# Optimization experiments

Measured on AMD Instinct MI355X. Metric: run time of the kernel, lower is better.

Reference implementation:

```python
import jax, jax.numpy as jnp
import numpy as np

EPS = 1e-8  # matches torch.nn.functional.cosine_similarity default eps


def setup_inputs() -> dict:
    key = jax.random.key(0)
    k1, k2 = jax.random.split(key)
    B, C, L, D = 65536, 64, 64, 128
    x = jax.random.normal(k1, (B, D), dtype=jnp.float32)
    category_embeddings = jax.random.normal(k2, (C, L, D), dtype=jnp.float32)
    leaf_usage_counts = jnp.zeros((C, L), dtype=jnp.float32)
    return {
        "x": x,
        "category_embeddings": category_embeddings,
        "leaf_usage_counts": leaf_usage_counts,
    }


def reference(x, category_embeddings, leaf_usage_counts):
    # Cosine similarity: [B, C, L] without materializing the broadcast [B,C,L,D].
    x_norm = jnp.maximum(jnp.linalg.norm(x, axis=-1, keepdims=True), EPS)        # [B, 1]
    e_norm = jnp.maximum(jnp.linalg.norm(category_embeddings, axis=-1), EPS)     # [C, L]
    dots = jnp.einsum('bd,cld->bcl', x, category_embeddings)                     # [B, C, L]
    cosine_sim = dots / (x_norm[:, :, None] * e_norm[None, :, :])                # [B, C, L]

    # Training-path usage-count update (done under no_grad in torch):
    # per-category bincount of argmax leaf, scatter-added into the buffer.
    max_indices = jnp.argmax(cosine_sim, axis=2)                                 # [B, C] int
    C, L = leaf_usage_counts.shape
    cat_ids = jnp.broadcast_to(jnp.arange(C)[None, :], max_indices.shape)        # [B, C]
    leaf_counts = jnp.zeros((C, L), jnp.float32).at[cat_ids, max_indices].add(1.0)
    new_leaf_usage_counts = leaf_usage_counts + leaf_counts                      # [C, L]

    cosine_sim_max = jnp.max(cosine_sim, axis=2)                                 # [B, C]
    return cosine_sim_max, new_leaf_usage_counts
```

## Files before the change

kernel.cpp:

```cpp
#include <hip/hip_runtime.h>
#include <stdint.h>
#include <stddef.h>

#define D      128
#define NCATS  64
#define NLEAF  64
#define NC_BLK 32
#define BM     256
#define BIAS   32.0f

typedef _Float16 half8_t  __attribute__((ext_vector_type(8)));
typedef _Float16 half4h_t __attribute__((ext_vector_type(4)));
typedef float    float4_t __attribute__((ext_vector_type(4)));

__device__ __forceinline__ void async_ld16(const void* g, void* l) {
  __builtin_amdgcn_global_load_lds((const __attribute__((address_space(1))) uint32_t*)g,
                                   (__attribute__((address_space(3))) uint32_t*)l,
                                   16, 0, 0);
}

#define UMAX(a, b) ((a) > (b) ? (a) : (b))
#define DPP_REDUCE16(p)                                                                   \
  do {                                                                                    \
    unsigned _t;                                                                          \
    _t = (unsigned)__builtin_amdgcn_mov_dpp((int)(p), 0x121, 0xf, 0xf, false); p = UMAX(p, _t); \
    _t = (unsigned)__builtin_amdgcn_mov_dpp((int)(p), 0x122, 0xf, 0xf, false); p = UMAX(p, _t); \
    _t = (unsigned)__builtin_amdgcn_mov_dpp((int)(p), 0x124, 0xf, 0xf, false); p = UMAX(p, _t); \
    _t = (unsigned)__builtin_amdgcn_mov_dpp((int)(p), 0x128, 0xf, 0xf, false); p = UMAX(p, _t); \
  } while (0)

__global__ __launch_bounds__(256) void prep_e_kernel(const float* __restrict__ e,
                                                     char* __restrict__ e16) {
  const int t  = threadIdx.x;
  const int rl = t >> 4;
  const int cc = t & 15;
  const int row = blockIdx.x * 16 + rl;
  const float* src = e + (size_t)row * D + cc * 8;
  float4_t v0 = *(const float4_t*)src;
  float4_t v1 = *(const float4_t*)(src + 4);
  float ss = v0.x*v0.x + v0.y*v0.y + v0.z*v0.z + v0.w*v0.w +
             v1.x*v1.x + v1.y*v1.y + v1.z*v1.z + v1.w*v1.w;
  ss += __shfl_xor(ss, 1);
  ss += __shfl_xor(ss, 2);
  ss += __shfl_xor(ss, 4);
  ss += __shfl_xor(ss, 8);
  const float inv = 1.0f / fmaxf(sqrtf(ss), 1e-8f);
  half8_t h;
  h[0] = (_Float16)(v0.x * inv); h[1] = (_Float16)(v0.y * inv);
  h[2] = (_Float16)(v0.z * inv); h[3] = (_Float16)(v0.w * inv);
  h[4] = (_Float16)(v1.x * inv); h[5] = (_Float16)(v1.y * inv);
  h[6] = (_Float16)(v1.z * inv); h[7] = (_Float16)(v1.w * inv);
  const int dc = cc ^ (rl & 7);
  *(half8_t*)(e16 + (size_t)row * 256 + dc * 16) = h;
}

__global__ __launch_bounds__(256) void init_counts_kernel(const float* __restrict__ in,
                                                          float* __restrict__ out) {
  const int i = blockIdx.x * 256 + threadIdx.x;
  out[i] = in[i];
}

__global__ __launch_bounds__(256, 2) void main_kernel(const float* __restrict__ x,
                                                      const char* __restrict__ e16,
                                                      float* __restrict__ cos_out,
                                                      float* __restrict__ counts_out) {
  __shared__ __align__(16) char ebuf[2][16384];
  __shared__ unsigned hist[NC_BLK * NLEAF];
  __shared__ _Float16 stage[BM * 36];

  const int tid  = threadIdx.x;
  const int w    = tid >> 6;
  const int lane = tid & 63;
  const int q    = lane >> 4;
  const int wl   = lane & 15;

  const int rb     = blockIdx.x >> 1;
  const int c_base = (blockIdx.x & 1) * NC_BLK;
  const int b_base = rb * BM;

  for (int i = tid; i < NC_BLK * NLEAF; i += 256) hist[i] = 0;

  {
    const char* g = e16 + (size_t)c_base * 16384 + w * 4096 + lane * 16;
    char* l = &ebuf[0][w * 4096 + lane * 16];
#pragma unroll
    for (int j = 0; j < 4; ++j) async_ld16(g + j * 1024, l + j * 1024);
  }

  half8_t a[4][4];
  float inv_x[4];
#pragma unroll
  for (int rt = 0; rt < 4; ++rt) {
    const int row = b_base + w * 64 + rt * 16 + wl;
    const float* xr = x + (size_t)row * D;
    float ss = 0.f;
#pragma unroll
    for (int s = 0; s < 4; ++s) {
      const float* p = xr + s * 32 + q * 8;
      float4_t v0 = *(const float4_t*)p;
      float4_t v1 = *(const float4_t*)(p + 4);
      half8_t h;
      h[0] = (_Float16)v0.x; h[1] = (_Float16)v0.y;
      h[2] = (_Float16)v0.z; h[3] = (_Float16)v0.w;
      h[4] = (_Float16)v1.x; h[5] = (_Float16)v1.y;
      h[6] = (_Float16)v1.z; h[7] = (_Float16)v1.w;
      a[rt][s] = h;
      ss += v0.x*v0.x + v0.y*v0.y + v0.z*v0.z + v0.w*v0.w +
            v1.x*v1.x + v1.y*v1.y + v1.z*v1.z + v1.w*v1.w;
    }
    ss += __shfl_xor(ss, 16);
    ss += __shfl_xor(ss, 32);
    inv_x[rt] = 1.0f / fmaxf(sqrtf(ss), 1e-8f);
  }

  int rowbase[4], xoff[4];
#pragma unroll
  for (int nt = 0; nt < 4; ++nt) rowbase[nt] = (nt * 16 + wl) * 256;
#pragma unroll
  for (int s = 0; s < 4; ++s) xoff[s] = ((q + 4 * s) ^ (wl & 7)) * 16;

  unsigned idxv[4];
#pragma unroll
  for (int nt = 0; nt < 4; ++nt) idxv[nt] = (unsigned)(nt * 16 + wl);

  const float4_t bias4 = {BIAS, BIAS, BIAS, BIAS};

  __syncthreads();

#pragma unroll 2
  for (int ci = 0; ci < NC_BLK; ++ci) {
    const int c = c_base + ci;
    const char* cur = ebuf[ci & 1];

    if (ci + 1 < NC_BLK) {
      const char* g = e16 + (size_t)(c + 1) * 16384 + w * 4096 + lane * 16;
      char* l = &ebuf[(ci + 1) & 1][w * 4096 + lane * 16];
#pragma unroll
      for (int j = 0; j < 4; ++j) async_ld16(g + j * 1024, l + j * 1024);
    }

    float4_t acc[4][4];
#pragma unroll
    for (int s = 0; s < 4; ++s) {
      half8_t b[4];
#pragma unroll
      for (int nt = 0; nt < 4; ++nt)
        b[nt] = *(const half8_t*)(cur + rowbase[nt] + xoff[s]);
#pragma unroll
      for (int rt = 0; rt < 4; ++rt)
#pragma unroll
        for (int nt = 0; nt < 4; ++nt)
          acc[rt][nt] = __builtin_amdgcn_mfma_f32_16x16x32_f16(
              a[rt][s], b[nt], (s == 0) ? bias4 : acc[rt][nt], 0, 0, 0);
    }

    unsigned pk[4][4];
#pragma unroll
    for (int rt = 0; rt < 4; ++rt) {
#pragma unroll
      for (int reg = 0; reg < 4; ++reg) {
        unsigned k0 = (__float_as_uint(acc[rt][0][reg]) & 0xFFFFFFC0u) | idxv[0];
        unsigned k1 = (__float_as_uint(acc[rt][1][reg]) & 0xFFFFFFC0u) | idxv[1];
        unsigned k2 = (__float_as_uint(acc[rt][2][reg]) & 0xFFFFFFC0u) | idxv[2];
        unsigned k3 = (__float_as_uint(acc[rt][3][reg]) & 0xFFFFFFC0u) | idxv[3];
        unsigned p = UMAX(UMAX(k0, k1), UMAX(k2, k3));
        DPP_REDUCE16(p);
        pk[rt][reg] = p;
      }
    }

    if ((wl >> 2) == q) {
      const int reg = wl & 3;
#pragma unroll
      for (int rt = 0; rt < 4; ++rt) {
        const unsigned p = pk[rt][reg];
        const float val = (__uint_as_float(p & 0xFFFFFFC0u) - BIAS) * inv_x[rt];
        stage[(w * 64 + rt * 16 + wl) * 36 + ci] = (_Float16)val;
        atomicAdd(&hist[ci * NLEAF + (int)(p & 63u)], 1u);
      }
    }
    __syncthreads();
  }

  __syncthreads();

#pragma unroll
  for (int k = 0; k < 8; ++k) {
    const int r  = (tid >> 3) + 32 * k;
    const int c0 = (tid & 7) * 4;
    half4h_t h = *(const half4h_t*)&stage[r * 36 + c0];
    float4_t v;
    v.x = (float)h[0]; v.y = (float)h[1]; v.z = (float)h[2]; v.w = (float)h[3];
    *(float4_t*)&cos_out[(size_t)(b_base + r) * NCATS + c_base + c0] = v;
  }

  for (int i = tid; i < NC_BLK * NLEAF; i += 256) {
    const unsigned v = hist[i];
    if (v) atomicAdd(&counts_out[c_base * NLEAF + i], (float)v);
  }
}

extern "C" void kernel_launch(void* const* d_in, const int* in_sizes, int n_in,
                              void* d_out, int out_size, void* d_ws, size_t ws_size,
                              hipStream_t stream) {
  const float* x   = (const float*)d_in[0];
  const float* e   = (const float*)d_in[1];
  const float* cin = (const float*)d_in[2];

  const int B = in_sizes[0] / D;
  const int erows = in_sizes[1] / D;
  float* cos_out = (float*)d_out;
  float* counts_out = cos_out + (size_t)B * NCATS;
  char* e16 = (char*)d_ws;

  prep_e_kernel<<<erows / 16, 256, 0, stream>>>(e, e16);
  init_counts_kernel<<<(NCATS * NLEAF) / 256, 256, 0, stream>>>(cin, counts_out);
  main_kernel<<<(B / BM) * 2, 256, 0, stream>>>(x, e16, cos_out, counts_out);
}
```

Before: 163.4 us.

## Load embedding fragments directly from global memory, split categories four ways, merge init kernel

The main kernel no longer double-buffers embedding tiles in LDS with async global-to-LDS loads and per-category barriers. Each lane now reads its B fragments straight from global memory, relying on L2/L1 caching of the small fp16 embedding table. Categories are split into four blocks of 16 per row tile, which doubles the grid and the number of times each x tile is loaded and converted. Dropping the big LDS buffer allows an occupancy hint of 3 blocks per CU, and the counts-copy kernel is folded into the prep kernel to save a launch.

```diff
diff --git a/kernel.cpp b/kernel.cpp
--- a/kernel.cpp
+++ b/kernel.cpp
@@ -5,19 +5,13 @@
 #define D      128
 #define NCATS  64
 #define NLEAF  64
-#define NC_BLK 32
+#define NC_BLK 16
 #define BM     256
 #define BIAS   32.0f
 
 typedef _Float16 half8_t  __attribute__((ext_vector_type(8)));
 typedef _Float16 half4h_t __attribute__((ext_vector_type(4)));
 typedef float    float4_t __attribute__((ext_vector_type(4)));
-
-__device__ __forceinline__ void async_ld16(const void* g, void* l) {
-  __builtin_amdgcn_global_load_lds((const __attribute__((address_space(1))) uint32_t*)g,
-                                   (__attribute__((address_space(3))) uint32_t*)l,
-                                   16, 0, 0);
-}
 
 #define UMAX(a, b) ((a) > (b) ? (a) : (b))
 #define DPP_REDUCE16(p)                                                                   \
@@ -30,7 +24,9 @@
   } while (0)
 
 __global__ __launch_bounds__(256) void prep_e_kernel(const float* __restrict__ e,
-                                                     char* __restrict__ e16) {
+                                                     char* __restrict__ e16,
+                                                     const float* __restrict__ cin,
+                                                     float* __restrict__ counts_out) {
   const int t  = threadIdx.x;
   const int rl = t >> 4;
   const int cc = t & 15;
@@ -50,23 +46,17 @@
   h[2] = (_Float16)(v0.z * inv); h[3] = (_Float16)(v0.w * inv);
   h[4] = (_Float16)(v1.x * inv); h[5] = (_Float16)(v1.y * inv);
   h[6] = (_Float16)(v1.z * inv); h[7] = (_Float16)(v1.w * inv);
-  const int dc = cc ^ (rl & 7);
-  *(half8_t*)(e16 + (size_t)row * 256 + dc * 16) = h;
+  *(half8_t*)(e16 + (size_t)row * 256 + cc * 16) = h;
+  if (blockIdx.x < (NCATS * NLEAF) / 256)
+    counts_out[blockIdx.x * 256 + t] = cin[blockIdx.x * 256 + t];
 }
 
-__global__ __launch_bounds__(256) void init_counts_kernel(const float* __restrict__ in,
-                                                          float* __restrict__ out) {
-  const int i = blockIdx.x * 256 + threadIdx.x;
-  out[i] = in[i];
-}
-
-__global__ __launch_bounds__(256, 2) void main_kernel(const float* __restrict__ x,
+__global__ __launch_bounds__(256, 3) void main_kernel(const float* __restrict__ x,
                                                       const char* __restrict__ e16,
                                                       float* __restrict__ cos_out,
                                                       float* __restrict__ counts_out) {
-  __shared__ __align__(16) char ebuf[2][16384];
   __shared__ unsigned hist[NC_BLK * NLEAF];
-  __shared__ _Float16 stage[BM * 36];
+  __shared__ __align__(16) _Float16 stage[BM * 20];
 
   const int tid  = threadIdx.x;
   const int w    = tid >> 6;
@@ -74,18 +64,11 @@
   const int q    = lane >> 4;
   const int wl   = lane & 15;
 
-  const int rb     = blockIdx.x >> 1;
-  const int c_base = (blockIdx.x & 1) * NC_BLK;
+  const int rb     = blockIdx.x >> 2;
+  const int c_base = (blockIdx.x & 3) * NC_BLK;
   const int b_base = rb * BM;
 
   for (int i = tid; i < NC_BLK * NLEAF; i += 256) hist[i] = 0;
-
-  {
-    const char* g = e16 + (size_t)c_base * 16384 + w * 4096 + lane * 16;
-    char* l = &ebuf[0][w * 4096 + lane * 16];
-#pragma unroll
-    for (int j = 0; j < 4; ++j) async_ld16(g + j * 1024, l + j * 1024);
-  }
 
   half8_t a[4][4];
   float inv_x[4];
@@ -113,39 +96,24 @@
     inv_x[rt] = 1.0f / fmaxf(sqrtf(ss), 1e-8f);
   }
 
-  int rowbase[4], xoff[4];
-#pragma unroll
-  for (int nt = 0; nt < 4; ++nt) rowbase[nt] = (nt * 16 + wl) * 256;
-#pragma unroll
-  for (int s = 0; s < 4; ++s) xoff[s] = ((q + 4 * s) ^ (wl & 7)) * 16;
-
   unsigned idxv[4];
 #pragma unroll
   for (int nt = 0; nt < 4; ++nt) idxv[nt] = (unsigned)(nt * 16 + wl);
 
   const float4_t bias4 = {BIAS, BIAS, BIAS, BIAS};
 
+  const char* ebase = e16 + (size_t)c_base * 16384 + wl * 256 + q * 16;
+
   __syncthreads();
 
-#pragma unroll 2
   for (int ci = 0; ci < NC_BLK; ++ci) {
-    const int c = c_base + ci;
-    const char* cur = ebuf[ci & 1];
-
-    if (ci + 1 < NC_BLK) {
-      const char* g = e16 + (size_t)(c + 1) * 16384 + w * 4096 + lane * 16;
-      char* l = &ebuf[(ci + 1) & 1][w * 4096 + lane * 16];
-#pragma unroll
-      for (int j = 0; j < 4; ++j) async_ld16(g + j * 1024, l + j * 1024);
-    }
-
     float4_t acc[4][4];
 #pragma unroll
     for (int s = 0; s < 4; ++s) {
       half8_t b[4];
 #pragma unroll
       for (int nt = 0; nt < 4; ++nt)
-        b[nt] = *(const half8_t*)(cur + rowbase[nt] + xoff[s]);
+        b[nt] = *(const half8_t*)(ebase + nt * 4096 + s * 64);
 #pragma unroll
       for (int rt = 0; rt < 4; ++rt)
 #pragma unroll
@@ -153,6 +121,7 @@
           acc[rt][nt] = __builtin_amdgcn_mfma_f32_16x16x32_f16(
               a[rt][s], b[nt], (s == 0) ? bias4 : acc[rt][nt], 0, 0, 0);
     }
+    ebase += 16384;
 
     unsigned pk[4][4];
 #pragma unroll
@@ -175,20 +144,20 @@
       for (int rt = 0; rt < 4; ++rt) {
         const unsigned p = pk[rt][reg];
         const float val = (__uint_as_float(p & 0xFFFFFFC0u) - BIAS) * inv_x[rt];
-        stage[(w * 64 + rt * 16 + wl) * 36 + ci] = (_Float16)val;
+        stage[(w * 64 + rt * 16 + wl) * 20 + ci] = (_Float16)val;
         atomicAdd(&hist[ci * NLEAF + (int)(p & 63u)], 1u);
       }
     }
-    __syncthreads();
   }
 
   __syncthreads();
 
 #pragma unroll
-  for (int k = 0; k < 8; ++k) {
-    const int r  = (tid >> 3) + 32 * k;
-    const int c0 = (tid & 7) * 4;
-    half4h_t h = *(const half4h_t*)&stage[r * 36 + c0];
+  for (int k = 0; k < 4; ++k) {
+    const int id = k * 256 + tid;
+    const int r  = id >> 2;
+    const int c0 = (id & 3) * 4;
+    half4h_t h = *(const half4h_t*)&stage[r * 20 + c0];
     float4_t v;
     v.x = (float)h[0]; v.y = (float)h[1]; v.z = (float)h[2]; v.w = (float)h[3];
     *(float4_t*)&cos_out[(size_t)(b_base + r) * NCATS + c_base + c0] = v;
@@ -213,7 +182,6 @@
   float* counts_out = cos_out + (size_t)B * NCATS;
   char* e16 = (char*)d_ws;
 
-  prep_e_kernel<<<erows / 16, 256, 0, stream>>>(e, e16);
-  init_counts_kernel<<<(NCATS * NLEAF) / 256, 256, 0, stream>>>(cin, counts_out);
-  main_kernel<<<(B / BM) * 2, 256, 0, stream>>>(x, e16, cos_out, counts_out);
+  prep_e_kernel<<<erows / 16, 256, 0, stream>>>(e, e16, cin, counts_out);
+  main_kernel<<<(B / BM) * (NCATS / NC_BLK), 256, 0, stream>>>(x, e16, cos_out, counts_out);
 }
```

Result: slower. 332.4 us (+103.5%).

## Split categories finer per block, shrink accumulators, and fuse count init into prep

Applied to the files above, without the earlier changes.

Each block now handles 8 categories instead of 32, so the grid grows fourfold. The GEMM loop now processes one N-tile at a time with a running max, which cuts live accumulator registers and allows launch bounds of 3 blocks per SIMD. The count-buffer initialization is folded into the prep kernel, removing one launch. The trade-off is that every x tile is reloaded and converted to fp16 eight times instead of twice, which adds global traffic and prologue work per block.

```diff
diff --git a/kernel.cpp b/kernel.cpp
--- a/kernel.cpp
+++ b/kernel.cpp
@@ -5,7 +5,7 @@
 #define D      128
 #define NCATS  64
 #define NLEAF  64
-#define NC_BLK 32
+#define NC_BLK 8
 #define BM     256
 #define BIAS   32.0f
 
@@ -30,7 +30,9 @@
   } while (0)
 
 __global__ __launch_bounds__(256) void prep_e_kernel(const float* __restrict__ e,
-                                                     char* __restrict__ e16) {
+                                                     char* __restrict__ e16,
+                                                     const float* __restrict__ cin,
+                                                     float* __restrict__ counts_out) {
   const int t  = threadIdx.x;
   const int rl = t >> 4;
   const int cc = t & 15;
@@ -52,21 +54,17 @@
   h[6] = (_Float16)(v1.z * inv); h[7] = (_Float16)(v1.w * inv);
   const int dc = cc ^ (rl & 7);
   *(half8_t*)(e16 + (size_t)row * 256 + dc * 16) = h;
-}
-
-__global__ __launch_bounds__(256) void init_counts_kernel(const float* __restrict__ in,
-                                                          float* __restrict__ out) {
-  const int i = blockIdx.x * 256 + threadIdx.x;
-  out[i] = in[i];
-}
-
-__global__ __launch_bounds__(256, 2) void main_kernel(const float* __restrict__ x,
+  if (blockIdx.x < (NCATS * NLEAF) / 256)
+    counts_out[blockIdx.x * 256 + t] = cin[blockIdx.x * 256 + t];
+}
+
+__global__ __launch_bounds__(256, 3) void main_kernel(const float* __restrict__ x,
                                                       const char* __restrict__ e16,
                                                       float* __restrict__ cos_out,
                                                       float* __restrict__ counts_out) {
   __shared__ __align__(16) char ebuf[2][16384];
   __shared__ unsigned hist[NC_BLK * NLEAF];
-  __shared__ _Float16 stage[BM * 36];
+  __shared__ __align__(16) _Float16 stage[BM * 12];
 
   const int tid  = threadIdx.x;
   const int w    = tid >> 6;
@@ -74,8 +72,8 @@
   const int q    = lane >> 4;
   const int wl   = lane & 15;
 
-  const int rb     = blockIdx.x >> 1;
-  const int c_base = (blockIdx.x & 1) * NC_BLK;
+  const int rb     = blockIdx.x >> 3;
+  const int c_base = (blockIdx.x & 7) * NC_BLK;
   const int b_base = rb * BM;
 
   for (int i = tid; i < NC_BLK * NLEAF; i += 256) hist[i] = 0;
@@ -119,55 +117,46 @@
 #pragma unroll
   for (int s = 0; s < 4; ++s) xoff[s] = ((q + 4 * s) ^ (wl & 7)) * 16;
 
-  unsigned idxv[4];
-#pragma unroll
-  for (int nt = 0; nt < 4; ++nt) idxv[nt] = (unsigned)(nt * 16 + wl);
-
   const float4_t bias4 = {BIAS, BIAS, BIAS, BIAS};
 
   __syncthreads();
 
-#pragma unroll 2
   for (int ci = 0; ci < NC_BLK; ++ci) {
-    const int c = c_base + ci;
     const char* cur = ebuf[ci & 1];
 
     if (ci + 1 < NC_BLK) {
-      const char* g = e16 + (size_t)(c + 1) * 16384 + w * 4096 + lane * 16;
+      const char* g = e16 + (size_t)(c_base + ci + 1) * 16384 + w * 4096 + lane * 16;
       char* l = &ebuf[(ci + 1) & 1][w * 4096 + lane * 16];
 #pragma unroll
       for (int j = 0; j < 4; ++j) async_ld16(g + j * 1024, l + j * 1024);
     }
 
-    float4_t acc[4][4];
-#pragma unroll
-    for (int s = 0; s < 4; ++s) {
-      half8_t b[4];
-#pragma unroll
-      for (int nt = 0; nt < 4; ++nt)
-        b[nt] = *(const half8_t*)(cur + rowbase[nt] + xoff[s]);
+    unsigned pk[4][4];
+#pragma unroll
+    for (int nt = 0; nt < 4; ++nt) {
+      float4_t acc[4];
+#pragma unroll
+      for (int s = 0; s < 4; ++s) {
+        half8_t b = *(const half8_t*)(cur + rowbase[nt] + xoff[s]);
+#pragma unroll
+        for (int rt = 0; rt < 4; ++rt)
+          acc[rt] = __builtin_amdgcn_mfma_f32_16x16x32_f16(
+              a[rt][s], b, (s == 0) ? bias4 : acc[rt], 0, 0, 0);
+      }
+      const unsigned idc = (unsigned)(nt * 16 + wl);
 #pragma unroll
       for (int rt = 0; rt < 4; ++rt)
 #pragma unroll
-        for (int nt = 0; nt < 4; ++nt)
-          acc[rt][nt] = __builtin_amdgcn_mfma_f32_16x16x32_f16(
-              a[rt][s], b[nt], (s == 0) ? bias4 : acc[rt][nt], 0, 0, 0);
-    }
-
-    unsigned pk[4][4];
-#pragma unroll
-    for (int rt = 0; rt < 4; ++rt) {
-#pragma unroll
-      for (int reg = 0; reg < 4; ++reg) {
-        unsigned k0 = (__float_as_uint(acc[rt][0][reg]) & 0xFFFFFFC0u) | idxv[0];
-        unsigned k1 = (__float_as_uint(acc[rt][1][reg]) & 0xFFFFFFC0u) | idxv[1];
-        unsigned k2 = (__float_as_uint(acc[rt][2][reg]) & 0xFFFFFFC0u) | idxv[2];
-        unsigned k3 = (__float_as_uint(acc[rt][3][reg]) & 0xFFFFFFC0u) | idxv[3];
-        unsigned p = UMAX(UMAX(k0, k1), UMAX(k2, k3));
-        DPP_REDUCE16(p);
-        pk[rt][reg] = p;
-      }
-    }
+        for (int reg = 0; reg < 4; ++reg) {
+          unsigned k = (__float_as_uint(acc[rt][reg]) & 0xFFFFFFC0u) | idc;
+          pk[rt][reg] = (nt == 0) ? k : UMAX(pk[rt][reg], k);
+        }
+    }
+
+#pragma unroll
+    for (int rt = 0; rt < 4; ++rt)
+#pragma unroll
+      for (int reg = 0; reg < 4; ++reg) DPP_REDUCE16(pk[rt][reg]);
 
     if ((wl >> 2) == q) {
       const int reg = wl & 3;
@@ -175,7 +164,7 @@
       for (int rt = 0; rt < 4; ++rt) {
         const unsigned p = pk[rt][reg];
         const float val = (__uint_as_float(p & 0xFFFFFFC0u) - BIAS) * inv_x[rt];
-        stage[(w * 64 + rt * 16 + wl) * 36 + ci] = (_Float16)val;
+        stage[(w * 64 + rt * 16 + wl) * 12 + ci] = (_Float16)val;
         atomicAdd(&hist[ci * NLEAF + (int)(p & 63u)], 1u);
       }
     }
@@ -185,10 +174,11 @@
   __syncthreads();
 
 #pragma unroll
-  for (int k = 0; k < 8; ++k) {
-    const int r  = (tid >> 3) + 32 * k;
-    const int c0 = (tid & 7) * 4;
-    half4h_t h = *(const half4h_t*)&stage[r * 36 + c0];
+  for (int k = 0; k < 2; ++k) {
+    const int id = k * 256 + tid;
+    const int r  = id >> 1;
+    const int c0 = (id & 1) * 4;
+    half4h_t h = *(const half4h_t*)&stage[r * 12 + c0];
     float4_t v;
     v.x = (float)h[0]; v.y = (float)h[1]; v.z = (float)h[2]; v.w = (float)h[3];
     *(float4_t*)&cos_out[(size_t)(b_base + r) * NCATS + c_base + c0] = v;
@@ -213,7 +203,6 @@
   float* counts_out = cos_out + (size_t)B * NCATS;
   char* e16 = (char*)d_ws;
 
-  prep_e_kernel<<<erows / 16, 256, 0, stream>>>(e, e16);
-  init_counts_kernel<<<(NCATS * NLEAF) / 256, 256, 0, stream>>>(cin, counts_out);
-  main_kernel<<<(B / BM) * 2, 256, 0, stream>>>(x, e16, cos_out, counts_out);
-}
+  prep_e_kernel<<<erows / 16, 256, 0, stream>>>(e, e16, cin, counts_out);
+  main_kernel<<<(B / BM) * (NCATS / NC_BLK), 256, 0, stream>>>(x, e16, cos_out, counts_out);
+}
```

Result: no change. 162.8 us (-0.3%).
